# Optimization experiments

Hardware: AMD Instinct MI355X
Metric: run time of the kernel (lower is better)

The kernel has to match this reference:

```python
import jax, jax.numpy as jnp
import numpy as np

B, S, E, H = 2, 2048, 1024, 16
D = E // H


def setup_inputs() -> dict:
    key = jax.random.key(0)
    ks = jax.random.split(key, 7)
    return {
        "query": jax.random.normal(ks[0], (B, S, E), dtype=jnp.float32),
        "key": jax.random.normal(ks[1], (B, S, E), dtype=jnp.float32),
        "value": jax.random.normal(ks[2], (B, S, E), dtype=jnp.float32),
        "Wq": jax.random.normal(ks[3], (E, E), dtype=jnp.float32) * (E ** -0.5),
        "Wk": jax.random.normal(ks[4], (E, E), dtype=jnp.float32) * (E ** -0.5),
        "Wv": jax.random.normal(ks[5], (E, E), dtype=jnp.float32) * (E ** -0.5),
        "Wo": jax.random.normal(ks[6], (E, E), dtype=jnp.float32) * (E ** -0.5),
    }


def reference(query, key, value, Wq, Wk, Wv, Wo):
    emb_dim = query.shape[-1]
    h = H
    d = emb_dim // h
    # QuantLinear with all-None quantizers == plain Linear (no bias):
    # torch Linear computes x @ W.T with W of shape [out, in].
    q = query @ Wq.T   # [b, s, e]
    k = key @ Wk.T
    v = value @ Wv.T
    # b s (h d) -> b h s d
    def split_heads(x):
        b, s, e = x.shape
        return x.reshape(b, s, h, d).transpose(0, 2, 1, 3)
    q = split_heads(q)
    k = split_heads(k)
    v = split_heads(v)
    # NOTE: faithful to source — scale uses full emb_dim, not head_dim.
    scale = emb_dim ** (-0.5)
    scores = jnp.einsum('bhsd,bhtd->bhst', q * scale, k)  # [b,h,s,s]
    weights = jax.nn.softmax(scores, axis=-1)  # QuantIdentity(None) == identity; dropout p=0
    heads = jnp.einsum('bhst,bhtd->bhsd', weights, v)
    # b h s d -> b s (h d)
    b = heads.shape[0]
    out = heads.transpose(0, 2, 1, 3).reshape(b, -1, emb_dim)
    return out @ Wo.T
```

## Files before the change

kernel.cpp:

```cpp
#include <hip/hip_runtime.h>
#include <hip/hip_bf16.h>
#include <stdint.h>

typedef __attribute__((ext_vector_type(8))) short s16x8;
typedef __attribute__((ext_vector_type(4))) float f32x4;

#define QSCALE 0.045084220027780106f

__device__ __forceinline__ unsigned short f2bf(float f) {
    union { float f; uint32_t u; } v; v.f = f;
    uint32_t u = v.u;
    u += 0x7FFFu + ((u >> 16) & 1u);
    return (unsigned short)(u >> 16);
}

__device__ __forceinline__ unsigned int pkbf2(float a, float b) {
    union { __hip_bfloat162 h; unsigned int u; } x;
    x.h = __float22bfloat162_rn(float2{a, b});
    return x.u;
}

#define GLOAD_LDS16(gptr, lptr)                                                         \
    __builtin_amdgcn_global_load_lds(                                                   \
        (const __attribute__((address_space(1))) unsigned int*)(gptr),                  \
        (__attribute__((address_space(3))) unsigned int*)(lptr), 16, 0, 0)

__global__ __launch_bounds__(256)
void cvt_all(const float* __restrict__ q, const float* __restrict__ k,
             const float* __restrict__ v, const float* __restrict__ wq,
             const float* __restrict__ wk, const float* __restrict__ wv,
             const float* __restrict__ wo,
             unsigned short* __restrict__ xq, unsigned short* __restrict__ xk,
             unsigned short* __restrict__ xv, unsigned short* __restrict__ wqb,
             unsigned short* __restrict__ wkb, unsigned short* __restrict__ wvb,
             unsigned short* __restrict__ wob)
{
    int bid = blockIdx.x;
    const float* src; unsigned short* dst; int rel;
    if (bid < 6144) {
        int s = bid >> 11; rel = bid & 2047;
        src = (s == 0) ? q : (s == 1) ? k : v;
        dst = (s == 0) ? xq : (s == 1) ? xk : xv;
    } else {
        int s = (bid - 6144) >> 9; rel = (bid - 6144) & 511;
        src = (s == 0) ? wq : (s == 1) ? wk : (s == 2) ? wv : wo;
        dst = (s == 0) ? wqb : (s == 1) ? wkb : (s == 2) ? wvb : wob;
    }
    size_t i = (size_t)rel * 256 + threadIdx.x;
    const float4* p = (const float4*)src;
    float4 a = p[i * 2];
    float4 b2 = p[i * 2 + 1];
    s16x8 r;
    r[0] = (short)f2bf(a.x);  r[1] = (short)f2bf(a.y);
    r[2] = (short)f2bf(a.z);  r[3] = (short)f2bf(a.w);
    r[4] = (short)f2bf(b2.x); r[5] = (short)f2bf(b2.y);
    r[6] = (short)f2bf(b2.z); r[7] = (short)f2bf(b2.w);
    *(s16x8*)(dst + i * 8) = r;
}

__device__ __forceinline__ void gemm_tile(const unsigned short* __restrict__ A,
                                          const unsigned short* __restrict__ Bt,
                                          void* __restrict__ C,
                                          int M, int N, int K, int f32out, float cscale,
                                          unsigned short* Al, unsigned short* Bl)
{
    const int tid  = threadIdx.x;
    const int lane = tid & 63;
    const int w    = tid >> 6;
    const int wr   = w >> 1, wc = w & 1;
    const int l15  = lane & 15, l4 = lane >> 4;

    const int m0 = blockIdx.x * 128;
    const int n0 = blockIdx.y * 128;

    f32x4 acc[4][4];
#pragma unroll
    for (int i = 0; i < 4; ++i)
#pragma unroll
        for (int j = 0; j < 4; ++j) acc[i][j] = (f32x4){0.f, 0.f, 0.f, 0.f};

    int srow[2], scol[2];
#pragma unroll
    for (int i = 0; i < 2; ++i) {
        int lin = (i * 4 + w) * 64 + lane;
        int row = lin >> 2;
        int u   = lin & 3;
        srow[i] = row;
        scol[i] = (u ^ ((row >> 1) & 3)) * 8;
    }
    int aoff[4], boff[4];
#pragma unroll
    for (int mi = 0; mi < 4; ++mi) {
        int rowa = wr * 64 + mi * 16 + l15;
        aoff[mi] = rowa * 32 + ((l4 ^ ((rowa >> 1) & 3)) * 8);
        int rowb = wc * 64 + mi * 16 + l15;
        boff[mi] = rowb * 32 + ((l4 ^ ((rowb >> 1) & 3)) * 8);
    }

    for (int k0 = 0; k0 < K; k0 += 32) {
#pragma unroll
        for (int i = 0; i < 2; ++i) {
            const unsigned short* gA = A + (size_t)(m0 + srow[i]) * K + k0 + scol[i];
            GLOAD_LDS16(gA, Al + (i * 4 + w) * 512);
            const unsigned short* gB = Bt + (size_t)(n0 + srow[i]) * K + k0 + scol[i];
            GLOAD_LDS16(gB, Bl + (i * 4 + w) * 512);
        }
        __syncthreads();
        s16x8 af[4], bfr[4];
#pragma unroll
        for (int mi = 0; mi < 4; ++mi) af[mi] = *(const s16x8*)(Al + aoff[mi]);
#pragma unroll
        for (int nf = 0; nf < 4; ++nf) bfr[nf] = *(const s16x8*)(Bl + boff[nf]);
#pragma unroll
        for (int mi = 0; mi < 4; ++mi)
#pragma unroll
            for (int nf = 0; nf < 4; ++nf)
                acc[mi][nf] = __builtin_amdgcn_mfma_f32_16x16x32_bf16(af[mi], bfr[nf], acc[mi][nf], 0, 0, 0);
        __syncthreads();
    }

#pragma unroll
    for (int mi = 0; mi < 4; ++mi)
#pragma unroll
        for (int nf = 0; nf < 4; ++nf)
#pragma unroll
            for (int r = 0; r < 4; ++r) {
                int row = m0 + wr * 64 + mi * 16 + l4 * 4 + r;
                int col = n0 + wc * 64 + nf * 16 + l15;
                float v = acc[mi][nf][r];
                if (f32out) ((float*)C)[(size_t)row * N + col] = v;
                else        ((unsigned short*)C)[(size_t)row * N + col] = f2bf(v * cscale);
            }
}

__global__ __launch_bounds__(256)
void gemm_qkv(const unsigned short* __restrict__ A0, const unsigned short* __restrict__ A1,
              const unsigned short* __restrict__ A2,
              const unsigned short* __restrict__ B0, const unsigned short* __restrict__ B1,
              const unsigned short* __restrict__ B2,
              unsigned short* __restrict__ C0, unsigned short* __restrict__ C1,
              unsigned short* __restrict__ C2)
{
    __shared__ unsigned short Al[128 * 32];
    __shared__ unsigned short Bl[128 * 32];
    int z = blockIdx.z;
    const unsigned short* A  = (z == 0) ? A0 : (z == 1) ? A1 : A2;
    const unsigned short* Bt = (z == 0) ? B0 : (z == 1) ? B1 : B2;
    unsigned short*       C  = (z == 0) ? C0 : (z == 1) ? C1 : C2;
    float cscale = (z == 0) ? QSCALE : 1.0f;
    gemm_tile(A, Bt, C, 4096, 1024, 1024, 0, cscale, Al, Bl);
}

__global__ __launch_bounds__(256)
void gemm_out(const unsigned short* __restrict__ A, const unsigned short* __restrict__ Bt,
              float* __restrict__ C)
{
    __shared__ unsigned short Al[128 * 32];
    __shared__ unsigned short Bl[128 * 32];
    gemm_tile(A, Bt, C, 4096, 1024, 1024, 1, 1.0f, Al, Bl);
}

__global__ __launch_bounds__(256)
void transpose_v(const unsigned short* __restrict__ Pv, unsigned short* __restrict__ Vt)
{
    __shared__ unsigned short T[64][72];
    const int t  = threadIdx.x;
    const int st = blockIdx.x, bh = blockIdx.y;
    const int b = bh >> 4, h = bh & 15;
    const int s0 = st * 64;
#pragma unroll
    for (int rp = 0; rp < 2; ++rp) {
        int sl = rp * 32 + (t >> 3);
        int dl = (t & 7) * 8;
        s16x8 v = *(const s16x8*)(Pv + (size_t)(b * 2048 + s0 + sl) * 1024 + h * 64 + dl);
        *(s16x8*)(&T[sl][dl]) = v;
    }
    __syncthreads();
#pragma unroll
    for (int rp = 0; rp < 2; ++rp) {
        int dl = rp * 32 + (t >> 3);
        int sl = (t & 7) * 8;
        s16x8 v;
#pragma unroll
        for (int j = 0; j < 8; ++j) v[j] = (short)T[sl + j][dl];
        *(s16x8*)(Vt + ((size_t)bh * 64 + dl) * 2048 + s0 + sl) = v;
    }
}

__global__ __launch_bounds__(256)
void attn4(const unsigned short* __restrict__ Q,
           const unsigned short* __restrict__ Kp,
           const unsigned short* __restrict__ Vt,
           unsigned short* __restrict__ O)
{
    __shared__ unsigned short Kl[2][2][64 * 64];
    __shared__ unsigned short Vl[2][2][64 * 64];
    __shared__ unsigned short Pl[4][2048];

    const int tid  = threadIdx.x;
    const int lane = tid & 63;
    const int w    = tid >> 6;
    const int l15  = lane & 15, l4 = lane >> 4;
    const int m7   = l15 & 7;

    const int hw  = blockIdx.x;
    const int xcd = hw & 7;
    const int idx = hw >> 3;
    const int bh  = xcd * 4 + (idx >> 4);
    const int qt  = idx & 15;
    const int b = bh >> 4, h = bh & 15;
    const int colbase = h * 64;

    s16x8 qf[2][2];
    size_t rowQg[2];
#pragma unroll
    for (int g = 0; g < 2; ++g) {
        rowQg[g] = (size_t)(b * 2048 + qt * 128 + w * 32 + g * 16 + l15);
#pragma unroll
        for (int kk = 0; kk < 2; ++kk)
            qf[g][kk] = *(const s16x8*)(Q + rowQg[g] * 1024 + colbase + kk * 32 + l4 * 8);
    }

    int krow[2], kcol[2];
#pragma unroll
    for (int i = 0; i < 2; ++i) {
        int lin = (i * 4 + w) * 64 + lane;
        krow[i] = lin >> 3;
        kcol[i] = ((lin & 7) ^ (krow[i] & 7)) * 8;
    }

    f32x4 o_acc[2][4];
#pragma unroll
    for (int g = 0; g < 2; ++g)
#pragma unroll
        for (int df = 0; df < 4; ++df) o_acc[g][df] = (f32x4){0.f, 0.f, 0.f, 0.f};
    float l_run[2] = {0.f, 0.f};

#define STAGE_KV(buf, kv0)                                                                     \
    {                                                                                          \
        _Pragma("unroll")                                                                      \
        for (int sub = 0; sub < 2; ++sub)                                                      \
        _Pragma("unroll")                                                                      \
        for (int i = 0; i < 2; ++i) {                                                          \
            const unsigned short* gk = Kp + (size_t)(b * 2048 + (kv0) + sub * 64 + krow[i])    \
                                          * 1024 + colbase + kcol[i];                          \
            GLOAD_LDS16(gk, &Kl[buf][sub][(i * 4 + w) * 512]);                                 \
            const unsigned short* gv = Vt + ((size_t)bh * 64 + krow[i]) * 2048                 \
                                          + (kv0) + sub * 64 + kcol[i];                        \
            GLOAD_LDS16(gv, &Vl[buf][sub][(i * 4 + w) * 512]);                                 \
        }                                                                                      \
    }

    STAGE_KV(0, 0);
    __syncthreads();

    for (int kt = 0; kt < 16; ++kt) {
        const int cur = kt & 1;
        if (kt < 15) STAGE_KV(cur ^ 1, (kt + 1) * 128);

#pragma unroll
        for (int sub = 0; sub < 2; ++sub) {
            f32x4 s[2][4];
#pragma unroll
            for (int g = 0; g < 2; ++g)
#pragma unroll
                for (int nf = 0; nf < 4; ++nf) s[g][nf] = (f32x4){0.f, 0.f, 0.f, 0.f};
#pragma unroll
            for (int kk = 0; kk < 2; ++kk) {
                const int sl = ((kk * 4 + l4) ^ m7) * 8;
#pragma unroll
                for (int nf = 0; nf < 4; ++nf) {
                    s16x8 kf = *(const s16x8*)(&Kl[cur][sub][(nf * 16 + l15) * 64 + sl]);
                    s[0][nf] = __builtin_amdgcn_mfma_f32_16x16x32_bf16(kf, qf[0][kk], s[0][nf], 0, 0, 0);
                    s[1][nf] = __builtin_amdgcn_mfma_f32_16x16x32_bf16(kf, qf[1][kk], s[1][nf], 0, 0, 0);
                }
            }

#pragma unroll
            for (int g = 0; g < 2; ++g) {
                float p[4][4];
                float ps = 0.f;
#pragma unroll
                for (int nf = 0; nf < 4; ++nf)
#pragma unroll
                    for (int r = 0; r < 4; ++r) {
                        p[nf][r] = __builtin_amdgcn_exp2f(s[g][nf][r]);
                        ps += p[nf][r];
                    }
                l_run[g] += ps;
#pragma unroll
                for (int nf = 0; nf < 4; ++nf) {
                    uint2 pw;
                    pw.x = pkbf2(p[nf][0], p[nf][1]);
                    pw.y = pkbf2(p[nf][2], p[nf][3]);
                    *(uint2*)(&Pl[w][(g * 16 + l15) * 64 + (((nf * 4 + l4) ^ (m7 << 1)) * 4)]) = pw;
                }
            }

            s16x8 pa[2][2];
#pragma unroll
            for (int g = 0; g < 2; ++g)
#pragma unroll
                for (int kk = 0; kk < 2; ++kk)
                    pa[g][kk] = *(const s16x8*)(&Pl[w][(g * 16 + l15) * 64 + (((kk * 4 + l4) ^ m7) * 8)]);

#pragma unroll
            for (int kk = 0; kk < 2; ++kk) {
                const int sl = ((kk * 4 + l4) ^ m7) * 8;
#pragma unroll
                for (int df = 0; df < 4; ++df) {
                    s16x8 vf = *(const s16x8*)(&Vl[cur][sub][(df * 16 + l15) * 64 + sl]);
                    o_acc[0][df] = __builtin_amdgcn_mfma_f32_16x16x32_bf16(vf, pa[0][kk], o_acc[0][df], 0, 0, 0);
                    o_acc[1][df] = __builtin_amdgcn_mfma_f32_16x16x32_bf16(vf, pa[1][kk], o_acc[1][df], 0, 0, 0);
                }
            }
        }
        __syncthreads();
    }

#pragma unroll
    for (int g = 0; g < 2; ++g) {
        float lsum = l_run[g];
        lsum += __shfl_xor(lsum, 16, 64);
        lsum += __shfl_xor(lsum, 32, 64);
        const float inv = 1.0f / lsum;
#pragma unroll
        for (int df = 0; df < 4; ++df) {
            uint2 pw;
            pw.x = pkbf2(o_acc[g][df][0] * inv, o_acc[g][df][1] * inv);
            pw.y = pkbf2(o_acc[g][df][2] * inv, o_acc[g][df][3] * inv);
            *(uint2*)(O + rowQg[g] * 1024 + colbase + df * 16 + l4 * 4) = pw;
        }
    }
#undef STAGE_KV
}

extern "C" void kernel_launch(void* const* d_in, const int* in_sizes, int n_in,
                              void* d_out, int out_size, void* d_ws, size_t ws_size,
                              hipStream_t stream)
{
    const float* query = (const float*)d_in[0];
    const float* key   = (const float*)d_in[1];
    const float* value = (const float*)d_in[2];
    const float* Wq    = (const float*)d_in[3];
    const float* Wk    = (const float*)d_in[4];
    const float* Wv    = (const float*)d_in[5];
    const float* Wo    = (const float*)d_in[6];
    float* out = (float*)d_out;

    char* ws = (char*)d_ws;
    const size_t SZX = (size_t)4096 * 1024 * 2;
    const size_t SZW = (size_t)1024 * 1024 * 2;
    unsigned short* Xq  = (unsigned short*)(ws + 0);
    unsigned short* Xk  = (unsigned short*)(ws + SZX);
    unsigned short* Xv  = (unsigned short*)(ws + 2 * SZX);
    unsigned short* Wqb = (unsigned short*)(ws + 3 * SZX);
    unsigned short* Wkb = (unsigned short*)(ws + 3 * SZX + SZW);
    unsigned short* Wvb = (unsigned short*)(ws + 3 * SZX + 2 * SZW);
    unsigned short* Wob = (unsigned short*)(ws + 3 * SZX + 3 * SZW);
    unsigned short* Pq  = (unsigned short*)(ws + 3 * SZX + 4 * SZW);
    unsigned short* Pk  = (unsigned short*)(ws + 4 * SZX + 4 * SZW);
    unsigned short* Pv  = (unsigned short*)(ws + 5 * SZX + 4 * SZW);
    unsigned short* AO  = (unsigned short*)(ws + 6 * SZX + 4 * SZW);
    unsigned short* Vt  = Xq;

    cvt_all<<<8192, 256, 0, stream>>>(query, key, value, Wq, Wk, Wv, Wo,
                                      Xq, Xk, Xv, Wqb, Wkb, Wvb, Wob);
    gemm_qkv<<<dim3(32, 8, 3), 256, 0, stream>>>(Xq, Xk, Xv, Wqb, Wkb, Wvb, Pq, Pk, Pv);
    transpose_v<<<dim3(32, 32), 256, 0, stream>>>(Pv, Vt);
    attn4<<<512, 256, 0, stream>>>(Pq, Pk, Vt, AO);
    gemm_out<<<dim3(32, 8, 1), 256, 0, stream>>>(AO, Wob, out);
}
```

Before: 135.3 us.

## Fuse V transpose into QKV GEMM epilogue and split attention KV across two wave groups

The V projection GEMM now writes its output directly in transposed [b,h,d,s] layout, which removes the separate transpose kernel and its extra round trip through global memory. The attention kernel moves to 512 threads. Two groups of four waves each process half of the key/value sequence for the same query tile, then combine their partial outputs and row sums through shared memory before normalising. This doubles the waves per query tile to improve latency hiding, at the cost of a final exchange and barrier. The transposed V stores are 8-byte scattered writes, which may coalesce less well.

```diff
diff --git a/kernel.cpp b/kernel.cpp
--- a/kernel.cpp
+++ b/kernel.cpp
@@ -61,7 +61,7 @@
 __device__ __forceinline__ void gemm_tile(const unsigned short* __restrict__ A,
                                           const unsigned short* __restrict__ Bt,
                                           void* __restrict__ C,
-                                          int M, int N, int K, int f32out, float cscale,
+                                          int M, int N, int K, int mode, float cscale,
                                           unsigned short* Al, unsigned short* Bl)
 {
     const int tid  = threadIdx.x;
@@ -122,15 +122,27 @@
 #pragma unroll
     for (int mi = 0; mi < 4; ++mi)
 #pragma unroll
-        for (int nf = 0; nf < 4; ++nf)
-#pragma unroll
-            for (int r = 0; r < 4; ++r) {
-                int row = m0 + wr * 64 + mi * 16 + l4 * 4 + r;
-                int col = n0 + wc * 64 + nf * 16 + l15;
-                float v = acc[mi][nf][r];
-                if (f32out) ((float*)C)[(size_t)row * N + col] = v;
-                else        ((unsigned short*)C)[(size_t)row * N + col] = f2bf(v * cscale);
-            }
+        for (int nf = 0; nf < 4; ++nf) {
+            if (mode == 2) {
+                int row0 = m0 + wr * 64 + mi * 16 + l4 * 4;
+                int colg = n0 + wc * 64 + nf * 16 + l15;
+                int vtrow = ((row0 >> 11) * 16 + (colg >> 6)) * 64 + (colg & 63);
+                int s0 = row0 & 2047;
+                uint2 pw;
+                pw.x = pkbf2(acc[mi][nf][0], acc[mi][nf][1]);
+                pw.y = pkbf2(acc[mi][nf][2], acc[mi][nf][3]);
+                *(uint2*)((unsigned short*)C + (size_t)vtrow * 2048 + s0) = pw;
+            } else {
+#pragma unroll
+                for (int r = 0; r < 4; ++r) {
+                    int row = m0 + wr * 64 + mi * 16 + l4 * 4 + r;
+                    int col = n0 + wc * 64 + nf * 16 + l15;
+                    float v = acc[mi][nf][r];
+                    if (mode == 1) ((float*)C)[(size_t)row * N + col] = v;
+                    else           ((unsigned short*)C)[(size_t)row * N + col] = f2bf(v * cscale);
+                }
+            }
+        }
 }
 
 __global__ __launch_bounds__(256)
@@ -148,7 +160,8 @@
     const unsigned short* Bt = (z == 0) ? B0 : (z == 1) ? B1 : B2;
     unsigned short*       C  = (z == 0) ? C0 : (z == 1) ? C1 : C2;
     float cscale = (z == 0) ? QSCALE : 1.0f;
-    gemm_tile(A, Bt, C, 4096, 1024, 1024, 0, cscale, Al, Bl);
+    int mode = (z == 2) ? 2 : 0;
+    gemm_tile(A, Bt, C, 4096, 1024, 1024, mode, cscale, Al, Bl);
 }
 
 __global__ __launch_bounds__(256)
@@ -160,46 +173,20 @@
     gemm_tile(A, Bt, C, 4096, 1024, 1024, 1, 1.0f, Al, Bl);
 }
 
-__global__ __launch_bounds__(256)
-void transpose_v(const unsigned short* __restrict__ Pv, unsigned short* __restrict__ Vt)
-{
-    __shared__ unsigned short T[64][72];
-    const int t  = threadIdx.x;
-    const int st = blockIdx.x, bh = blockIdx.y;
-    const int b = bh >> 4, h = bh & 15;
-    const int s0 = st * 64;
-#pragma unroll
-    for (int rp = 0; rp < 2; ++rp) {
-        int sl = rp * 32 + (t >> 3);
-        int dl = (t & 7) * 8;
-        s16x8 v = *(const s16x8*)(Pv + (size_t)(b * 2048 + s0 + sl) * 1024 + h * 64 + dl);
-        *(s16x8*)(&T[sl][dl]) = v;
-    }
-    __syncthreads();
-#pragma unroll
-    for (int rp = 0; rp < 2; ++rp) {
-        int dl = rp * 32 + (t >> 3);
-        int sl = (t & 7) * 8;
-        s16x8 v;
-#pragma unroll
-        for (int j = 0; j < 8; ++j) v[j] = (short)T[sl + j][dl];
-        *(s16x8*)(Vt + ((size_t)bh * 64 + dl) * 2048 + s0 + sl) = v;
-    }
-}
-
-__global__ __launch_bounds__(256)
-void attn4(const unsigned short* __restrict__ Q,
+__global__ __launch_bounds__(512, 4)
+void attn5(const unsigned short* __restrict__ Q,
            const unsigned short* __restrict__ Kp,
            const unsigned short* __restrict__ Vt,
            unsigned short* __restrict__ O)
 {
     __shared__ unsigned short Kl[2][2][64 * 64];
     __shared__ unsigned short Vl[2][2][64 * 64];
-    __shared__ unsigned short Pl[4][2048];
+    __shared__ unsigned short Pl[8][1024];
 
     const int tid  = threadIdx.x;
     const int lane = tid & 63;
     const int w    = tid >> 6;
+    const int half = w >> 2, ws = w & 3;
     const int l15  = lane & 15, l4 = lane >> 4;
     const int m7   = l15 & 7;
 
@@ -210,12 +197,13 @@
     const int qt  = idx & 15;
     const int b = bh >> 4, h = bh & 15;
     const int colbase = h * 64;
+    const int kvbase = half * 1024;
 
     s16x8 qf[2][2];
     size_t rowQg[2];
 #pragma unroll
     for (int g = 0; g < 2; ++g) {
-        rowQg[g] = (size_t)(b * 2048 + qt * 128 + w * 32 + g * 16 + l15);
+        rowQg[g] = (size_t)(b * 2048 + qt * 128 + ws * 32 + g * 16 + l15);
 #pragma unroll
         for (int kk = 0; kk < 2; ++kk)
             qf[g][kk] = *(const s16x8*)(Q + rowQg[g] * 1024 + colbase + kk * 32 + l4 * 8);
@@ -224,7 +212,7 @@
     int krow[2], kcol[2];
 #pragma unroll
     for (int i = 0; i < 2; ++i) {
-        int lin = (i * 4 + w) * 64 + lane;
+        int lin = (i * 4 + ws) * 64 + lane;
         krow[i] = lin >> 3;
         kcol[i] = ((lin & 7) ^ (krow[i] & 7)) * 8;
     }
@@ -239,97 +227,113 @@
 #define STAGE_KV(buf, kv0)                                                                     \
     {                                                                                          \
         _Pragma("unroll")                                                                      \
-        for (int sub = 0; sub < 2; ++sub)                                                      \
-        _Pragma("unroll")                                                                      \
         for (int i = 0; i < 2; ++i) {                                                          \
-            const unsigned short* gk = Kp + (size_t)(b * 2048 + (kv0) + sub * 64 + krow[i])    \
-                                          * 1024 + colbase + kcol[i];                          \
-            GLOAD_LDS16(gk, &Kl[buf][sub][(i * 4 + w) * 512]);                                 \
+            const unsigned short* gk = Kp + (size_t)(b * 2048 + (kv0) + krow[i]) * 1024        \
+                                          + colbase + kcol[i];                                 \
+            GLOAD_LDS16(gk, &Kl[half][buf][(i * 4 + ws) * 512]);                               \
             const unsigned short* gv = Vt + ((size_t)bh * 64 + krow[i]) * 2048                 \
-                                          + (kv0) + sub * 64 + kcol[i];                        \
-            GLOAD_LDS16(gv, &Vl[buf][sub][(i * 4 + w) * 512]);                                 \
+                                          + (kv0) + kcol[i];                                   \
+            GLOAD_LDS16(gv, &Vl[half][buf][(i * 4 + ws) * 512]);                               \
         }                                                                                      \
     }
 
-    STAGE_KV(0, 0);
+    STAGE_KV(0, kvbase);
     __syncthreads();
 
     for (int kt = 0; kt < 16; ++kt) {
         const int cur = kt & 1;
-        if (kt < 15) STAGE_KV(cur ^ 1, (kt + 1) * 128);
-
-#pragma unroll
-        for (int sub = 0; sub < 2; ++sub) {
-            f32x4 s[2][4];
-#pragma unroll
-            for (int g = 0; g < 2; ++g)
-#pragma unroll
-                for (int nf = 0; nf < 4; ++nf) s[g][nf] = (f32x4){0.f, 0.f, 0.f, 0.f};
-#pragma unroll
-            for (int kk = 0; kk < 2; ++kk) {
-                const int sl = ((kk * 4 + l4) ^ m7) * 8;
-#pragma unroll
-                for (int nf = 0; nf < 4; ++nf) {
-                    s16x8 kf = *(const s16x8*)(&Kl[cur][sub][(nf * 16 + l15) * 64 + sl]);
-                    s[0][nf] = __builtin_amdgcn_mfma_f32_16x16x32_bf16(kf, qf[0][kk], s[0][nf], 0, 0, 0);
-                    s[1][nf] = __builtin_amdgcn_mfma_f32_16x16x32_bf16(kf, qf[1][kk], s[1][nf], 0, 0, 0);
+        if (kt < 15) STAGE_KV(cur ^ 1, kvbase + (kt + 1) * 64);
+
+        f32x4 s[2][4];
+#pragma unroll
+        for (int g = 0; g < 2; ++g)
+#pragma unroll
+            for (int nf = 0; nf < 4; ++nf) s[g][nf] = (f32x4){0.f, 0.f, 0.f, 0.f};
+#pragma unroll
+        for (int kk = 0; kk < 2; ++kk) {
+            const int sl = ((kk * 4 + l4) ^ m7) * 8;
+#pragma unroll
+            for (int nf = 0; nf < 4; ++nf) {
+                s16x8 kf = *(const s16x8*)(&Kl[half][cur][(nf * 16 + l15) * 64 + sl]);
+                s[0][nf] = __builtin_amdgcn_mfma_f32_16x16x32_bf16(kf, qf[0][kk], s[0][nf], 0, 0, 0);
+                s[1][nf] = __builtin_amdgcn_mfma_f32_16x16x32_bf16(kf, qf[1][kk], s[1][nf], 0, 0, 0);
+            }
+        }
+
+        s16x8 pa[2][2];
+#pragma unroll
+        for (int g = 0; g < 2; ++g) {
+            float p[4][4];
+            float ps = 0.f;
+#pragma unroll
+            for (int nf = 0; nf < 4; ++nf)
+#pragma unroll
+                for (int r = 0; r < 4; ++r) {
+                    p[nf][r] = __builtin_amdgcn_exp2f(s[g][nf][r]);
+                    ps += p[nf][r];
                 }
-            }
-
-#pragma unroll
-            for (int g = 0; g < 2; ++g) {
-                float p[4][4];
-                float ps = 0.f;
-#pragma unroll
-                for (int nf = 0; nf < 4; ++nf)
-#pragma unroll
-                    for (int r = 0; r < 4; ++r) {
-                        p[nf][r] = __builtin_amdgcn_exp2f(s[g][nf][r]);
-                        ps += p[nf][r];
-                    }
-                l_run[g] += ps;
-#pragma unroll
-                for (int nf = 0; nf < 4; ++nf) {
-                    uint2 pw;
-                    pw.x = pkbf2(p[nf][0], p[nf][1]);
-                    pw.y = pkbf2(p[nf][2], p[nf][3]);
-                    *(uint2*)(&Pl[w][(g * 16 + l15) * 64 + (((nf * 4 + l4) ^ (m7 << 1)) * 4)]) = pw;
-                }
-            }
-
-            s16x8 pa[2][2];
-#pragma unroll
-            for (int g = 0; g < 2; ++g)
-#pragma unroll
-                for (int kk = 0; kk < 2; ++kk)
-                    pa[g][kk] = *(const s16x8*)(&Pl[w][(g * 16 + l15) * 64 + (((kk * 4 + l4) ^ m7) * 8)]);
-
-#pragma unroll
-            for (int kk = 0; kk < 2; ++kk) {
-                const int sl = ((kk * 4 + l4) ^ m7) * 8;
-#pragma unroll
-                for (int df = 0; df < 4; ++df) {
-                    s16x8 vf = *(const s16x8*)(&Vl[cur][sub][(df * 16 + l15) * 64 + sl]);
-                    o_acc[0][df] = __builtin_amdgcn_mfma_f32_16x16x32_bf16(vf, pa[0][kk], o_acc[0][df], 0, 0, 0);
-                    o_acc[1][df] = __builtin_amdgcn_mfma_f32_16x16x32_bf16(vf, pa[1][kk], o_acc[1][df], 0, 0, 0);
-                }
+            l_run[g] += ps;
+#pragma unroll
+            for (int nf = 0; nf < 4; ++nf) {
+                uint2 pw;
+                pw.x = pkbf2(p[nf][0], p[nf][1]);
+                pw.y = pkbf2(p[nf][2], p[nf][3]);
+                *(uint2*)(&Pl[w][l15 * 64 + (((nf * 4 + l4) ^ (m7 << 1)) * 4)]) = pw;
+            }
+#pragma unroll
+            for (int kk = 0; kk < 2; ++kk)
+                pa[g][kk] = *(const s16x8*)(&Pl[w][l15 * 64 + (((kk * 4 + l4) ^ m7) * 8)]);
+        }
+
+#pragma unroll
+        for (int kk = 0; kk < 2; ++kk) {
+            const int sl = ((kk * 4 + l4) ^ m7) * 8;
+#pragma unroll
+            for (int df = 0; df < 4; ++df) {
+                s16x8 vf = *(const s16x8*)(&Vl[half][cur][(df * 16 + l15) * 64 + sl]);
+                o_acc[0][df] = __builtin_amdgcn_mfma_f32_16x16x32_bf16(vf, pa[0][kk], o_acc[0][df], 0, 0, 0);
+                o_acc[1][df] = __builtin_amdgcn_mfma_f32_16x16x32_bf16(vf, pa[1][kk], o_acc[1][df], 0, 0, 0);
             }
         }
         __syncthreads();
     }
 
+    float lsum[2];
 #pragma unroll
     for (int g = 0; g < 2; ++g) {
-        float lsum = l_run[g];
-        lsum += __shfl_xor(lsum, 16, 64);
-        lsum += __shfl_xor(lsum, 32, 64);
-        const float inv = 1.0f / lsum;
-#pragma unroll
-        for (int df = 0; df < 4; ++df) {
-            uint2 pw;
-            pw.x = pkbf2(o_acc[g][df][0] * inv, o_acc[g][df][1] * inv);
-            pw.y = pkbf2(o_acc[g][df][2] * inv, o_acc[g][df][3] * inv);
-            *(uint2*)(O + rowQg[g] * 1024 + colbase + df * 16 + l4 * 4) = pw;
+        lsum[g] = l_run[g];
+        lsum[g] += __shfl_xor(lsum[g], 16, 64);
+        lsum[g] += __shfl_xor(lsum[g], 32, 64);
+    }
+
+    f32x4* Xch = (f32x4*)&Kl[0][0][0];
+    float* Lx  = (float*)&Vl[0][0][0];
+
+    if (half == 1) {
+#pragma unroll
+        for (int g = 0; g < 2; ++g)
+#pragma unroll
+            for (int df = 0; df < 4; ++df)
+                Xch[((ws * 8 + g * 4 + df) << 6) + lane] = o_acc[g][df];
+        if (l4 == 0) {
+            Lx[(ws * 2 + 0) * 16 + l15] = lsum[0];
+            Lx[(ws * 2 + 1) * 16 + l15] = lsum[1];
+        }
+    }
+    __syncthreads();
+    if (half == 0) {
+#pragma unroll
+        for (int g = 0; g < 2; ++g) {
+            float lt = lsum[g] + Lx[(ws * 2 + g) * 16 + l15];
+            const float inv = 1.0f / lt;
+#pragma unroll
+            for (int df = 0; df < 4; ++df) {
+                f32x4 po = Xch[((ws * 8 + g * 4 + df) << 6) + lane];
+                uint2 pw;
+                pw.x = pkbf2((o_acc[g][df][0] + po[0]) * inv, (o_acc[g][df][1] + po[1]) * inv);
+                pw.y = pkbf2((o_acc[g][df][2] + po[2]) * inv, (o_acc[g][df][3] + po[3]) * inv);
+                *(uint2*)(O + rowQg[g] * 1024 + colbase + df * 16 + l4 * 4) = pw;
+            }
         }
     }
 #undef STAGE_KV
@@ -360,14 +364,12 @@
     unsigned short* Wob = (unsigned short*)(ws + 3 * SZX + 3 * SZW);
     unsigned short* Pq  = (unsigned short*)(ws + 3 * SZX + 4 * SZW);
     unsigned short* Pk  = (unsigned short*)(ws + 4 * SZX + 4 * SZW);
-    unsigned short* Pv  = (unsigned short*)(ws + 5 * SZX + 4 * SZW);
+    unsigned short* Vt  = (unsigned short*)(ws + 5 * SZX + 4 * SZW);
     unsigned short* AO  = (unsigned short*)(ws + 6 * SZX + 4 * SZW);
-    unsigned short* Vt  = Xq;
 
     cvt_all<<<8192, 256, 0, stream>>>(query, key, value, Wq, Wk, Wv, Wo,
                                       Xq, Xk, Xv, Wqb, Wkb, Wvb, Wob);
-    gemm_qkv<<<dim3(32, 8, 3), 256, 0, stream>>>(Xq, Xk, Xv, Wqb, Wkb, Wvb, Pq, Pk, Pv);
-    transpose_v<<<dim3(32, 32), 256, 0, stream>>>(Pv, Vt);
-    attn4<<<512, 256, 0, stream>>>(Pq, Pk, Vt, AO);
+    gemm_qkv<<<dim3(32, 8, 3), 256, 0, stream>>>(Xq, Xk, Xv, Wqb, Wkb, Wvb, Pq, Pk, Vt);
+    attn5<<<512, 512, 0, stream>>>(Pq, Pk, Vt, AO);
     gemm_out<<<dim3(32, 8, 1), 256, 0, stream>>>(AO, Wob, out);
 }
```

New measurement: 136.0 us. About the same (+0.5%).

## Split attention KV range across two wave groups using 32x32 MFMA

Applied to the files above, without the earlier changes.

Replaces the attention kernel with a 512-thread version in which two groups of four waves each process half of the key/value sequence for the same query tile, then combine partial outputs and row sums through shared memory. It switches from 16x16x32 to 32x32x16 bf16 MFMA tiles. The P operand is now rearranged in registers with cross-lane shuffles instead of a round trip through shared memory. This is meant to raise parallelism per block, remove the P LDS traffic and improve MFMA efficiency, at the cost of a final cross-group reduction and higher register pressure.

```diff
diff --git a/kernel.cpp b/kernel.cpp
--- a/kernel.cpp
+++ b/kernel.cpp
@@ -4,6 +4,7 @@
 
 typedef __attribute__((ext_vector_type(8))) short s16x8;
 typedef __attribute__((ext_vector_type(4))) float f32x4;
+typedef __attribute__((ext_vector_type(16))) float f32x16;
 
 #define QSCALE 0.045084220027780106f
 
@@ -187,150 +188,150 @@
     }
 }
 
-__global__ __launch_bounds__(256)
-void attn4(const unsigned short* __restrict__ Q,
+__global__ __launch_bounds__(512, 4)
+void attn6(const unsigned short* __restrict__ Q,
            const unsigned short* __restrict__ Kp,
            const unsigned short* __restrict__ Vt,
            unsigned short* __restrict__ O)
 {
     __shared__ unsigned short Kl[2][2][64 * 64];
     __shared__ unsigned short Vl[2][2][64 * 64];
-    __shared__ unsigned short Pl[4][2048];
 
     const int tid  = threadIdx.x;
     const int lane = tid & 63;
     const int w    = tid >> 6;
-    const int l15  = lane & 15, l4 = lane >> 4;
-    const int m7   = l15 & 7;
+    const int half = w >> 2, ws = w & 3;
+    const int q31  = lane & 31;
+    const int lh   = lane >> 5;
+    const int m7q  = q31 & 7;
 
     const int hw  = blockIdx.x;
     const int xcd = hw & 7;
     const int idx = hw >> 3;
     const int bh  = xcd * 4 + (idx >> 4);
     const int qt  = idx & 15;
-    const int b = bh >> 4, h = bh & 15;
-    const int colbase = h * 64;
-
-    s16x8 qf[2][2];
-    size_t rowQg[2];
-#pragma unroll
-    for (int g = 0; g < 2; ++g) {
-        rowQg[g] = (size_t)(b * 2048 + qt * 128 + w * 32 + g * 16 + l15);
-#pragma unroll
-        for (int kk = 0; kk < 2; ++kk)
-            qf[g][kk] = *(const s16x8*)(Q + rowQg[g] * 1024 + colbase + kk * 32 + l4 * 8);
-    }
+    const int b = bh >> 4, hd = bh & 15;
+    const int colbase = hd * 64;
+    const int kvbase = half * 1024;
+
+    const size_t qrow = (size_t)(b * 2048 + qt * 128 + ws * 32 + q31);
+    s16x8 qf[4];
+#pragma unroll
+    for (int dk = 0; dk < 4; ++dk)
+        qf[dk] = *(const s16x8*)(Q + qrow * 1024 + colbase + dk * 16 + lh * 8);
 
     int krow[2], kcol[2];
 #pragma unroll
     for (int i = 0; i < 2; ++i) {
-        int lin = (i * 4 + w) * 64 + lane;
+        int lin = (i * 4 + ws) * 64 + lane;
         krow[i] = lin >> 3;
         kcol[i] = ((lin & 7) ^ (krow[i] & 7)) * 8;
     }
 
-    f32x4 o_acc[2][4];
-#pragma unroll
-    for (int g = 0; g < 2; ++g)
-#pragma unroll
-        for (int df = 0; df < 4; ++df) o_acc[g][df] = (f32x4){0.f, 0.f, 0.f, 0.f};
-    float l_run[2] = {0.f, 0.f};
+    f32x16 oa[2] = {};
+    float l_run = 0.f;
 
 #define STAGE_KV(buf, kv0)                                                                     \
     {                                                                                          \
         _Pragma("unroll")                                                                      \
-        for (int sub = 0; sub < 2; ++sub)                                                      \
-        _Pragma("unroll")                                                                      \
         for (int i = 0; i < 2; ++i) {                                                          \
-            const unsigned short* gk = Kp + (size_t)(b * 2048 + (kv0) + sub * 64 + krow[i])    \
-                                          * 1024 + colbase + kcol[i];                          \
-            GLOAD_LDS16(gk, &Kl[buf][sub][(i * 4 + w) * 512]);                                 \
+            const unsigned short* gk = Kp + (size_t)(b * 2048 + (kv0) + krow[i]) * 1024        \
+                                          + colbase + kcol[i];                                 \
+            GLOAD_LDS16(gk, &Kl[half][buf][(i * 4 + ws) * 512]);                               \
             const unsigned short* gv = Vt + ((size_t)bh * 64 + krow[i]) * 2048                 \
-                                          + (kv0) + sub * 64 + kcol[i];                        \
-            GLOAD_LDS16(gv, &Vl[buf][sub][(i * 4 + w) * 512]);                                 \
+                                          + (kv0) + kcol[i];                                   \
+            GLOAD_LDS16(gv, &Vl[half][buf][(i * 4 + ws) * 512]);                               \
         }                                                                                      \
     }
 
-    STAGE_KV(0, 0);
+    STAGE_KV(0, kvbase);
     __syncthreads();
 
     for (int kt = 0; kt < 16; ++kt) {
         const int cur = kt & 1;
-        if (kt < 15) STAGE_KV(cur ^ 1, (kt + 1) * 128);
-
-#pragma unroll
-        for (int sub = 0; sub < 2; ++sub) {
-            f32x4 s[2][4];
-#pragma unroll
-            for (int g = 0; g < 2; ++g)
-#pragma unroll
-                for (int nf = 0; nf < 4; ++nf) s[g][nf] = (f32x4){0.f, 0.f, 0.f, 0.f};
-#pragma unroll
-            for (int kk = 0; kk < 2; ++kk) {
-                const int sl = ((kk * 4 + l4) ^ m7) * 8;
-#pragma unroll
-                for (int nf = 0; nf < 4; ++nf) {
-                    s16x8 kf = *(const s16x8*)(&Kl[cur][sub][(nf * 16 + l15) * 64 + sl]);
-                    s[0][nf] = __builtin_amdgcn_mfma_f32_16x16x32_bf16(kf, qf[0][kk], s[0][nf], 0, 0, 0);
-                    s[1][nf] = __builtin_amdgcn_mfma_f32_16x16x32_bf16(kf, qf[1][kk], s[1][nf], 0, 0, 0);
-                }
-            }
-
-#pragma unroll
-            for (int g = 0; g < 2; ++g) {
-                float p[4][4];
-                float ps = 0.f;
-#pragma unroll
-                for (int nf = 0; nf < 4; ++nf)
-#pragma unroll
-                    for (int r = 0; r < 4; ++r) {
-                        p[nf][r] = __builtin_amdgcn_exp2f(s[g][nf][r]);
-                        ps += p[nf][r];
-                    }
-                l_run[g] += ps;
-#pragma unroll
-                for (int nf = 0; nf < 4; ++nf) {
-                    uint2 pw;
-                    pw.x = pkbf2(p[nf][0], p[nf][1]);
-                    pw.y = pkbf2(p[nf][2], p[nf][3]);
-                    *(uint2*)(&Pl[w][(g * 16 + l15) * 64 + (((nf * 4 + l4) ^ (m7 << 1)) * 4)]) = pw;
-                }
-            }
-
-            s16x8 pa[2][2];
-#pragma unroll
-            for (int g = 0; g < 2; ++g)
-#pragma unroll
-                for (int kk = 0; kk < 2; ++kk)
-                    pa[g][kk] = *(const s16x8*)(&Pl[w][(g * 16 + l15) * 64 + (((kk * 4 + l4) ^ m7) * 8)]);
-
-#pragma unroll
-            for (int kk = 0; kk < 2; ++kk) {
-                const int sl = ((kk * 4 + l4) ^ m7) * 8;
-#pragma unroll
-                for (int df = 0; df < 4; ++df) {
-                    s16x8 vf = *(const s16x8*)(&Vl[cur][sub][(df * 16 + l15) * 64 + sl]);
-                    o_acc[0][df] = __builtin_amdgcn_mfma_f32_16x16x32_bf16(vf, pa[0][kk], o_acc[0][df], 0, 0, 0);
-                    o_acc[1][df] = __builtin_amdgcn_mfma_f32_16x16x32_bf16(vf, pa[1][kk], o_acc[1][df], 0, 0, 0);
-                }
-            }
+        if (kt < 15) STAGE_KV(cur ^ 1, kvbase + (kt + 1) * 64);
+
+        f32x16 s0 = {}, s1 = {};
+#pragma unroll
+        for (int dk = 0; dk < 4; ++dk) {
+            const int sl = ((dk * 2 + lh) ^ m7q) * 8;
+            s16x8 kf0 = *(const s16x8*)(&Kl[half][cur][q31 * 64 + sl]);
+            s16x8 kf1 = *(const s16x8*)(&Kl[half][cur][(32 + q31) * 64 + sl]);
+            s0 = __builtin_amdgcn_mfma_f32_32x32x16_bf16(kf0, qf[dk], s0, 0, 0, 0);
+            s1 = __builtin_amdgcn_mfma_f32_32x32x16_bf16(kf1, qf[dk], s1, 0, 0, 0);
+        }
+
+        unsigned int PK[2][8];
+        float ps = 0.f;
+        {
+            float p[16];
+#pragma unroll
+            for (int i = 0; i < 16; ++i) { p[i] = __builtin_amdgcn_exp2f(s0[i]); ps += p[i]; }
+#pragma unroll
+            for (int j = 0; j < 8; ++j) PK[0][j] = pkbf2(p[2 * j], p[2 * j + 1]);
+#pragma unroll
+            for (int i = 0; i < 16; ++i) { p[i] = __builtin_amdgcn_exp2f(s1[i]); ps += p[i]; }
+#pragma unroll
+            for (int j = 0; j < 8; ++j) PK[1][j] = pkbf2(p[2 * j], p[2 * j + 1]);
+        }
+        l_run += ps;
+
+#pragma unroll
+        for (int t = 0; t < 4; ++t) {
+            const int bk = t >> 1, j0 = (t & 1) * 4;
+            unsigned int A0 = PK[bk][j0],     C0 = PK[bk][j0 + 2];
+            unsigned int A1 = PK[bk][j0 + 1], C1 = PK[bk][j0 + 3];
+            unsigned int sA0 = (unsigned int)__shfl_xor((int)A0, 32, 64);
+            unsigned int sC0 = (unsigned int)__shfl_xor((int)C0, 32, 64);
+            unsigned int sA1 = (unsigned int)__shfl_xor((int)A1, 32, 64);
+            unsigned int sC1 = (unsigned int)__shfl_xor((int)C1, 32, 64);
+            union { unsigned int u[4]; s16x8 v; } pa;
+            pa.u[0] = lh ? sC0 : A0;
+            pa.u[1] = lh ? sC1 : A1;
+            pa.u[2] = lh ? C0 : sA0;
+            pa.u[3] = lh ? C1 : sA1;
+            const int slv = ((t * 2 + lh) ^ m7q) * 8;
+            s16x8 vf0 = *(const s16x8*)(&Vl[half][cur][q31 * 64 + slv]);
+            s16x8 vf1 = *(const s16x8*)(&Vl[half][cur][(32 + q31) * 64 + slv]);
+            oa[0] = __builtin_amdgcn_mfma_f32_32x32x16_bf16(vf0, pa.v, oa[0], 0, 0, 0);
+            oa[1] = __builtin_amdgcn_mfma_f32_32x32x16_bf16(vf1, pa.v, oa[1], 0, 0, 0);
         }
         __syncthreads();
     }
 
-#pragma unroll
-    for (int g = 0; g < 2; ++g) {
-        float lsum = l_run[g];
-        lsum += __shfl_xor(lsum, 16, 64);
-        lsum += __shfl_xor(lsum, 32, 64);
-        const float inv = 1.0f / lsum;
-#pragma unroll
-        for (int df = 0; df < 4; ++df) {
-            uint2 pw;
-            pw.x = pkbf2(o_acc[g][df][0] * inv, o_acc[g][df][1] * inv);
-            pw.y = pkbf2(o_acc[g][df][2] * inv, o_acc[g][df][3] * inv);
-            *(uint2*)(O + rowQg[g] * 1024 + colbase + df * 16 + l4 * 4) = pw;
-        }
+    l_run += __shfl_xor(l_run, 32, 64);
+
+    f32x4* Xch = (f32x4*)&Kl[0][0][0];
+    float*  Lx = (float*)&Vl[0][0][0];
+
+    if (half == 1) {
+#pragma unroll
+        for (int dh = 0; dh < 2; ++dh)
+#pragma unroll
+            for (int rg = 0; rg < 4; ++rg) {
+                f32x4 c = { oa[dh][rg * 4 + 0], oa[dh][rg * 4 + 1],
+                            oa[dh][rg * 4 + 2], oa[dh][rg * 4 + 3] };
+                Xch[((ws * 8 + dh * 4 + rg) << 6) + lane] = c;
+            }
+        if (lh == 0) Lx[ws * 32 + q31] = l_run;
+    }
+    __syncthreads();
+    if (half == 0) {
+        const float lt  = l_run + Lx[ws * 32 + q31];
+        const float inv = 1.0f / lt;
+#pragma unroll
+        for (int dh = 0; dh < 2; ++dh)
+#pragma unroll
+            for (int rg = 0; rg < 4; ++rg) {
+                f32x4 po = Xch[((ws * 8 + dh * 4 + rg) << 6) + lane];
+                const int d0 = dh * 32 + rg * 8 + lh * 4;
+                uint2 pw;
+                pw.x = pkbf2((oa[dh][rg * 4 + 0] + po[0]) * inv,
+                             (oa[dh][rg * 4 + 1] + po[1]) * inv);
+                pw.y = pkbf2((oa[dh][rg * 4 + 2] + po[2]) * inv,
+                             (oa[dh][rg * 4 + 3] + po[3]) * inv);
+                *(uint2*)(O + qrow * 1024 + colbase + d0) = pw;
+            }
     }
 #undef STAGE_KV
 }
@@ -368,6 +369,6 @@
                                       Xq, Xk, Xv, Wqb, Wkb, Wvb, Wob);
     gemm_qkv<<<dim3(32, 8, 3), 256, 0, stream>>>(Xq, Xk, Xv, Wqb, Wkb, Wvb, Pq, Pk, Pv);
     transpose_v<<<dim3(32, 32), 256, 0, stream>>>(Pv, Vt);
-    attn4<<<512, 256, 0, stream>>>(Pq, Pk, Vt, AO);
+    attn6<<<512, 512, 0, stream>>>(Pq, Pk, Vt, AO);
     gemm_out<<<dim3(32, 8, 1), 256, 0, stream>>>(AO, Wob, out);
 }
```

Result: faster. 132.4 us (-2.2%).
